# Performance work log

Hardware: AMD Instinct MI355X
Metric: run time of the kernel (lower is better)

## Reference

```python
import jax, jax.numpy as jnp
import numpy as np


def _lstm(x, W_ih, W_hh, b_ih, b_hh):
    """PyTorch-convention LSTM. x: [B, T, I] -> (ys [B, T, H], h_T [B, H]).
    Gate order i, f, g, o as in torch.nn.LSTM."""
    def step(carry, xt):
        h, c = carry
        gates = xt @ W_ih.T + b_ih + h @ W_hh.T + b_hh
        i, f, g, o = jnp.split(gates, 4, axis=-1)
        c = jax.nn.sigmoid(f) * c + jax.nn.sigmoid(i) * jnp.tanh(g)
        h = jax.nn.sigmoid(o) * jnp.tanh(c)
        return (h, c), h
    B = x.shape[0]
    H = W_hh.shape[1]
    init = (jnp.zeros((B, H), x.dtype), jnp.zeros((B, H), x.dtype))
    (hT, _), ys = jax.lax.scan(step, init, jnp.swapaxes(x, 0, 1))
    return jnp.swapaxes(ys, 0, 1), hT


def setup_inputs():
    key = jax.random.key(0)
    ks = jax.random.split(key, 13)
    B, S, F = 256, 1024, 16
    p = lambda k, shape: jax.random.normal(k, shape, jnp.float32) * 0.1
    return {
        "x": jax.random.normal(ks[0], (B, S, F), jnp.float32),
        "data": 0,
        "W_ih1": p(ks[1], (32, 1)),  "W_hh1": p(ks[2], (32, 8)),
        "b_ih1": p(ks[3], (32,)),    "b_hh1": p(ks[4], (32,)),
        "W_ih2": p(ks[5], (512, 8)), "W_hh2": p(ks[6], (512, 128)),
        "b_ih2": p(ks[7], (512,)),   "b_hh2": p(ks[8], (512,)),
        "W1": p(ks[9], (64, 128)),   "b1": p(ks[10], (64,)),
        "W2": p(ks[11], (1, 64)),    "b2": p(ks[12], (1,)),
    }


def reference(x, data, W_ih1, W_hh1, b_ih1, b_hh1,
              W_ih2, W_hh2, b_ih2, b_hh2, W1, b1, W2, b2):
    B, S, F = x.shape
    # rnn1: original loops over batch; here all B*S rows are one big batch of
    # length-F sequences with feature dim 1. We only need the final hidden h_T.
    x1 = x.reshape(B * S, F, 1)
    _, h1 = _lstm(x1, W_ih1, W_hh1, b_ih1, b_hh1)            # [B*S, 8]
    # original does .detach().numpy() -> gradient is cut here
    h1 = jax.lax.stop_gradient(h1).reshape(B, S, 8)
    ys2, _ = _lstm(h1, W_ih2, W_hh2, b_ih2, b_hh2)           # [B, S, 128]
    last = ys2[:, -1, :]                                     # [B, 128]
    return (last @ W1.T + b1) @ W2.T + b2                    # [B, 1]
```

## Files before the change

kernel.cpp:

```cpp
#include <hip/hip_runtime.h>
#include <cstdint>

typedef _Float16 f16x2 __attribute__((ext_vector_type(2)));

#define L2E 1.44269504f

__device__ __forceinline__ float sig2(float y) {
  return __builtin_amdgcn_rcpf(1.f + exp2f(-y));
}
__device__ __forceinline__ float tanhc(float c) {
  return fmaf(2.f, __builtin_amdgcn_rcpf(1.f + exp2f(c * (-2.f * L2E))), -1.f);
}
__device__ __forceinline__ int packf16(float a, float b) {
  f16x2 p; p.x = (_Float16)a; p.y = (_Float16)b;
  return __builtin_bit_cast(int, p);
}
__device__ __forceinline__ float dot2(int w, int h, float acc) {
  return __builtin_amdgcn_fdot2(__builtin_bit_cast(f16x2, w),
                                __builtin_bit_cast(f16x2, h), acc, false);
}
template <int CTRL>
__device__ __forceinline__ float qp(float v) {
  return __int_as_float(__builtin_amdgcn_update_dpp(
      0, __float_as_int(v), CTRL, 0xF, 0xF, true));
}
#define QP_X1 0xB1

__global__ __launch_bounds__(256, 1) void fused_kernel(
    const float* __restrict__ x, const float* __restrict__ Wih1,
    const float* __restrict__ Whh1, const float* __restrict__ bih1,
    const float* __restrict__ bhh1, const float* __restrict__ Wih2,
    const float* __restrict__ Whh2, const float* __restrict__ bih2,
    const float* __restrict__ bhh2, const float* __restrict__ Wd1,
    const float* __restrict__ bd1, const float* __restrict__ Wd2,
    const float* __restrict__ bd2, float* __restrict__ out) {
  __shared__ __align__(16) int4 sX[1026];
  __shared__ __align__(16) _Float16 sH[2][128];

  const int b = blockIdx.x;
  const int t = threadIdx.x;

  {
    int whh2[128];
#pragma unroll
    for (int r = 0; r < 32; ++r) {
      const float s = (r >> 3) == 2 ? 2.f * L2E : L2E;
#pragma unroll
      for (int j = 0; j < 4; ++j) {
        float2 v = ((const float2*)(Whh1 + r * 8))[j];
        whh2[r * 4 + j] = packf16(v.x * s, v.y * s);
      }
    }
    int wxb[32];
#pragma unroll
    for (int r = 0; r < 32; ++r) {
      const float s = (r >> 3) == 2 ? 2.f * L2E : L2E;
      wxb[r] = packf16(Wih1[r] * s, (bih1[r] + bhh1[r]) * s);
    }
#pragma unroll
    for (int i = 0; i < 128; i += 8)
      asm volatile("" : "+v"(whh2[i]), "+v"(whh2[i + 1]), "+v"(whh2[i + 2]),
                        "+v"(whh2[i + 3]), "+v"(whh2[i + 4]), "+v"(whh2[i + 5]),
                        "+v"(whh2[i + 6]), "+v"(whh2[i + 7]));

#pragma unroll 1
    for (int ch = 0; ch < 4; ++ch) {
      const int c = ch * 256 + t;
      const float* __restrict__ xp = x + ((size_t)b * 1024 + c) * 16;
      float cc[8];
      int h2[4];
#pragma unroll
      for (int k = 0; k < 8; ++k) cc[k] = 0.f;
#pragma unroll
      for (int j = 0; j < 4; ++j) h2[j] = 0;

      float xv = xp[0];
#pragma unroll 1
      for (int u = 0; u < 16; ++u) {
        float xnl = xp[(u + 1) & 15];
        const int xt1 = packf16(xv, 1.f);
        float hn[8];
#pragma unroll
        for (int k = 0; k < 8; ++k) {
          float acc[4];
#pragma unroll
          for (int gi = 0; gi < 4; ++gi) {
            const int r = gi * 8 + k;
            float a = dot2(wxb[r], xt1, 0.f);
            a = dot2(whh2[r * 4 + 0], h2[0], a);
            a = dot2(whh2[r * 4 + 1], h2[1], a);
            a = dot2(whh2[r * 4 + 2], h2[2], a);
            a = dot2(whh2[r * 4 + 3], h2[3], a);
            acc[gi] = a;
          }
          float iv = sig2(acc[0]), fv = sig2(acc[1]);
          float gv = fmaf(2.f, sig2(acc[2]), -1.f), ov = sig2(acc[3]);
          cc[k] = fmaf(fv, cc[k], iv * gv);
          hn[k] = ov * tanhc(cc[k]);
        }
#pragma unroll
        for (int j = 0; j < 4; ++j) h2[j] = packf16(hn[2 * j], hn[2 * j + 1]);
        xv = xnl;
      }
      int4 o;
      o.x = h2[0]; o.y = h2[1]; o.z = h2[2]; o.w = h2[3];
      sX[c] = o;
    }
  }

  const int m = t >> 1;
  const int q = t & 1;
  const bool isq1 = (q == 1);

  int w[128];
#pragma unroll
  for (int g = 0; g < 4; ++g) {
    const float s = (g == 2) ? 2.f * L2E : L2E;
    const float2* p = (const float2*)(Whh2 + (size_t)(g * 128 + m) * 128 + q * 64);
#pragma unroll
    for (int j = 0; j < 32; ++j) {
      float2 v = p[j];
      w[g * 32 + j] = packf16(v.x * s, v.y * s);
    }
  }
#pragma unroll
  for (int i = 0; i < 128; i += 8)
    asm volatile("" : "+v"(w[i]), "+v"(w[i + 1]), "+v"(w[i + 2]),
                      "+v"(w[i + 3]), "+v"(w[i + 4]), "+v"(w[i + 5]),
                      "+v"(w[i + 6]), "+v"(w[i + 7]));

  int wigA[4], wigB[4];
  float biasA, biasB;
  {
    const int gA = 2 * q, gB = 2 * q + 1;
    const float sa = (gA == 2) ? 2.f * L2E : L2E;
    const float sb = L2E;
    const int rowA = gA * 128 + m;
    const int rowB = gB * 128 + m;
    const float2* pa = (const float2*)(Wih2 + (size_t)rowA * 8);
    const float2* pb = (const float2*)(Wih2 + (size_t)rowB * 8);
#pragma unroll
    for (int j = 0; j < 4; ++j) {
      float2 va = pa[j], vb = pb[j];
      wigA[j] = packf16(va.x * sa, va.y * sa);
      wigB[j] = packf16(vb.x * sb, vb.y * sb);
    }
    biasA = (bih2[rowA] + bhh2[rowA]) * sa;
    biasB = (bih2[rowB] + bhh2[rowB]) * sb;
  }

  int hq[32];
#pragma unroll
  for (int i = 0; i < 32; ++i) hq[i] = 0;
  float c = 0.f;

  __syncthreads();
  int4 xc = sX[0];

#define LSTM2_STEP(BUF, NEXT_IDX)                                          \
  {                                                                        \
    float bxA = biasA, bxB = biasB;                                        \
    bxA = dot2(wigA[0], xc.x, bxA);                                        \
    bxA = dot2(wigA[1], xc.y, bxA);                                        \
    bxA = dot2(wigA[2], xc.z, bxA);                                        \
    bxA = dot2(wigA[3], xc.w, bxA);                                        \
    bxB = dot2(wigB[0], xc.x, bxB);                                        \
    bxB = dot2(wigB[1], xc.y, bxB);                                        \
    bxB = dot2(wigB[2], xc.z, bxB);                                        \
    bxB = dot2(wigB[3], xc.w, bxB);                                        \
    float R0a = 0.f, R1a = 0.f, R2a = 0.f, R3a = 0.f;                      \
    float R0b = 0.f, R1b = 0.f, R2b = 0.f, R3b = 0.f;                      \
    _Pragma("unroll")                                                      \
    for (int j = 0; j < 16; ++j) {                                         \
      R0a = dot2(w[j], hq[j], R0a);                                        \
      R1a = dot2(w[32 + j], hq[j], R1a);                                   \
      R2a = dot2(w[64 + j], hq[j], R2a);                                   \
      R3a = dot2(w[96 + j], hq[j], R3a);                                   \
    }                                                                      \
    _Pragma("unroll")                                                      \
    for (int j = 16; j < 32; ++j) {                                        \
      R0b = dot2(w[j], hq[j], R0b);                                        \
      R1b = dot2(w[32 + j], hq[j], R1b);                                   \
      R2b = dot2(w[64 + j], hq[j], R2b);                                   \
      R3b = dot2(w[96 + j], hq[j], R3b);                                   \
    }                                                                      \
    float R0 = R0a + R0b, R1 = R1a + R1b;                                  \
    float R2 = R2a + R2b, R3 = R3a + R3b;                                  \
    float vA = isq1 ? R0 : R2;                                             \
    float Sa = (isq1 ? R2 : R0) + qp<QP_X1>(vA) + bxA;                     \
    float vB = isq1 ? R1 : R3;                                             \
    float Sb = (isq1 ? R3 : R1) + qp<QP_X1>(vB) + bxB;                     \
    float sga = sig2(Sa);                                                  \
    float actA = isq1 ? fmaf(2.f, sga, -1.f) : sga;                        \
    float actB = sig2(Sb);                                                 \
    float ga = qp<QP_X1>(actA);                                            \
    float gb = qp<QP_X1>(actB);                                            \
    float iv = isq1 ? ga : actA;                                           \
    float gv = isq1 ? actA : ga;                                           \
    float fv = isq1 ? gb : actB;                                           \
    float ov = isq1 ? actB : gb;                                           \
    c = fmaf(fv, c, iv * gv);                                              \
    float hx = ov * tanhc(c);                                              \
    if (!isq1) sH[BUF][m] = (_Float16)hx;                                  \
    __syncthreads();                                                       \
    const int4* src = (const int4*)(&sH[BUF][q * 64]);                     \
    int4 A = src[0], Bv = src[1], C = src[2], D = src[3];                  \
    int4 E = src[4], F = src[5], G2 = src[6], H = src[7];                  \
    hq[0] = A.x;   hq[1] = A.y;   hq[2] = A.z;   hq[3] = A.w;              \
    hq[4] = Bv.x;  hq[5] = Bv.y;  hq[6] = Bv.z;  hq[7] = Bv.w;             \
    hq[8] = C.x;   hq[9] = C.y;   hq[10] = C.z;  hq[11] = C.w;             \
    hq[12] = D.x;  hq[13] = D.y;  hq[14] = D.z;  hq[15] = D.w;             \
    hq[16] = E.x;  hq[17] = E.y;  hq[18] = E.z;  hq[19] = E.w;             \
    hq[20] = F.x;  hq[21] = F.y;  hq[22] = F.z;  hq[23] = F.w;             \
    hq[24] = G2.x; hq[25] = G2.y; hq[26] = G2.z; hq[27] = G2.w;            \
    hq[28] = H.x;  hq[29] = H.y;  hq[30] = H.z;  hq[31] = H.w;             \
    xc = sX[NEXT_IDX];                                                     \
  }

#pragma unroll 1
  for (int ts2 = 0; ts2 < 512; ++ts2) {
    LSTM2_STEP(0, 2 * ts2 + 1)
    LSTM2_STEP(1, 2 * ts2 + 2)
  }
#undef LSTM2_STEP

  if (t < 64) {
    float a = bd1[t];
#pragma unroll
    for (int k = 0; k < 128; ++k)
      a = fmaf(Wd1[t * 128 + k], (float)sH[1][k], a);
    float v = a * Wd2[t];
#pragma unroll
    for (int off = 32; off > 0; off >>= 1) v += __shfl_down(v, off);
    if (t == 0) out[b] = v + bd2[0];
  }
}

extern "C" void kernel_launch(void* const* d_in, const int* in_sizes, int n_in,
                              void* d_out, int out_size, void* d_ws, size_t ws_size,
                              hipStream_t stream) {
  const float* x    = (const float*)d_in[0];
  const float* Wih1 = (const float*)d_in[2];
  const float* Whh1 = (const float*)d_in[3];
  const float* bih1 = (const float*)d_in[4];
  const float* bhh1 = (const float*)d_in[5];
  const float* Wih2 = (const float*)d_in[6];
  const float* Whh2 = (const float*)d_in[7];
  const float* bih2 = (const float*)d_in[8];
  const float* bhh2 = (const float*)d_in[9];
  const float* W1   = (const float*)d_in[10];
  const float* b1   = (const float*)d_in[11];
  const float* W2   = (const float*)d_in[12];
  const float* b2   = (const float*)d_in[13];
  float* out = (float*)d_out;

  fused_kernel<<<256, 256, 0, stream>>>(x, Wih1, Whh1, bih1, bhh1,
                                        Wih2, Whh2, bih2, bhh2,
                                        W1, b1, W2, b2, out);
}
```

Baseline: 659.3 us.

## Pack two batch sequences per 512-thread block, halving the grid

Each block now processes two batch elements with 512 threads, each 256-thread half running its own LSTM2 recurrence on separate shared-memory buffers. The grid shrinks from 256 to 128 blocks. The aim is better use of each CU, since 256 blocks on a 256-CU device left one wave group per CU and latency-bound. The risk is that the shared __syncthreads now couples both halves across all 512 threads, so every step's barrier costs more and one half can stall the other.

Measured after the change: 1.081 ms. 1.64x slower.

```diff
diff --git a/kernel.cpp b/kernel.cpp
--- a/kernel.cpp
+++ b/kernel.cpp
@@ -26,7 +26,7 @@
 }
 #define QP_X1 0xB1
 
-__global__ __launch_bounds__(256, 1) void fused_kernel(
+__global__ __launch_bounds__(512, 1) void fused_kernel(
     const float* __restrict__ x, const float* __restrict__ Wih1,
     const float* __restrict__ Whh1, const float* __restrict__ bih1,
     const float* __restrict__ bhh1, const float* __restrict__ Wih2,
@@ -34,8 +34,8 @@
     const float* __restrict__ bhh2, const float* __restrict__ Wd1,
     const float* __restrict__ bd1, const float* __restrict__ Wd2,
     const float* __restrict__ bd2, float* __restrict__ out) {
-  __shared__ __align__(16) int4 sX[1026];
-  __shared__ __align__(16) _Float16 sH[2][128];
+  __shared__ __align__(16) int4 sX2[2][1026];
+  __shared__ __align__(16) _Float16 sH2[2][2][128];
 
   const int b = blockIdx.x;
   const int t = threadIdx.x;
@@ -65,8 +65,8 @@
 
 #pragma unroll 1
     for (int ch = 0; ch < 4; ++ch) {
-      const int c = ch * 256 + t;
-      const float* __restrict__ xp = x + ((size_t)b * 1024 + c) * 16;
+      const int c = ch * 512 + t;
+      const float* __restrict__ xp = x + ((size_t)b * 2048 + c) * 16;
       float cc[8];
       int h2[4];
 #pragma unroll
@@ -104,12 +104,14 @@
       }
       int4 o;
       o.x = h2[0]; o.y = h2[1]; o.z = h2[2]; o.w = h2[3];
-      sX[c] = o;
-    }
-  }
-
-  const int m = t >> 1;
-  const int q = t & 1;
+      sX2[c >> 10][c & 1023] = o;
+    }
+  }
+
+  const int sq = t >> 8;
+  const int tl = t & 255;
+  const int m = tl >> 1;
+  const int q = tl & 1;
   const bool isq1 = (q == 1);
 
   int w[128];
@@ -154,8 +156,11 @@
   for (int i = 0; i < 32; ++i) hq[i] = 0;
   float c = 0.f;
 
+  const int4* __restrict__ sXs = sX2[sq];
+  _Float16 (* __restrict__ sHs)[128] = sH2[sq];
+
   __syncthreads();
-  int4 xc = sX[0];
+  int4 xc = sXs[0];
 
 #define LSTM2_STEP(BUF, NEXT_IDX)                                          \
   {                                                                        \
@@ -201,9 +206,9 @@
     float ov = isq1 ? actB : gb;                                           \
     c = fmaf(fv, c, iv * gv);                                              \
     float hx = ov * tanhc(c);                                              \
-    if (!isq1) sH[BUF][m] = (_Float16)hx;                                  \
+    if (!isq1) sHs[BUF][m] = (_Float16)hx;                                 \
     __syncthreads();                                                       \
-    const int4* src = (const int4*)(&sH[BUF][q * 64]);                     \
+    const int4* src = (const int4*)(&sHs[BUF][q * 64]);                    \
     int4 A = src[0], Bv = src[1], C = src[2], D = src[3];                  \
     int4 E = src[4], F = src[5], G2 = src[6], H = src[7];                  \
     hq[0] = A.x;   hq[1] = A.y;   hq[2] = A.z;   hq[3] = A.w;              \
@@ -214,7 +219,7 @@
     hq[20] = F.x;  hq[21] = F.y;  hq[22] = F.z;  hq[23] = F.w;             \
     hq[24] = G2.x; hq[25] = G2.y; hq[26] = G2.z; hq[27] = G2.w;            \
     hq[28] = H.x;  hq[29] = H.y;  hq[30] = H.z;  hq[31] = H.w;             \
-    xc = sX[NEXT_IDX];                                                     \
+    xc = sXs[NEXT_IDX];                                                    \
   }
 
 #pragma unroll 1
@@ -224,15 +229,15 @@
   }
 #undef LSTM2_STEP
 
-  if (t < 64) {
-    float a = bd1[t];
+  if (tl < 64) {
+    float a = bd1[tl];
 #pragma unroll
     for (int k = 0; k < 128; ++k)
-      a = fmaf(Wd1[t * 128 + k], (float)sH[1][k], a);
-    float v = a * Wd2[t];
+      a = fmaf(Wd1[tl * 128 + k], (float)sHs[1][k], a);
+    float v = a * Wd2[tl];
 #pragma unroll
     for (int off = 32; off > 0; off >>= 1) v += __shfl_down(v, off);
-    if (t == 0) out[b] = v + bd2[0];
+    if (tl == 0) out[2 * b + sq] = v + bd2[0];
   }
 }
 
@@ -254,7 +259,7 @@
   const float* b2   = (const float*)d_in[13];
   float* out = (float*)d_out;
 
-  fused_kernel<<<256, 256, 0, stream>>>(x, Wih1, Whh1, bih1, bhh1,
+  fused_kernel<<<128, 512, 0, stream>>>(x, Wih1, Whh1, bih1, bhh1,
                                         Wih2, Whh2, bih2, bhh2,
                                         W1, b1, W2, b2, out);
 }
```

## Split LSTM2 hidden units across 4 lanes with fp32 FMA and 512 threads

Applied to the files above, without the earlier changes.

Doubles the block to 512 threads. Each hidden unit of the second LSTM is now handled by 4 lanes, each covering 32 of the 128 hidden inputs for all four gates, with a two-level DPP quad reduction and an exchange of the gate values. The packed fp16 dot2 path is replaced by fp32 FMAs, and h and the layer-1 outputs are stored in shared memory as fp32. This halves the serial per-step dot work on each lane, at the cost of more shuffles, a larger block taking part in each barrier, and more LDS traffic. Layer 1 now runs in 2 chunks instead of 4.

New measurement: 832.0 us. 26.2% more time.

```diff
diff --git a/kernel.cpp b/kernel.cpp
--- a/kernel.cpp
+++ b/kernel.cpp
@@ -25,8 +25,9 @@
       0, __float_as_int(v), CTRL, 0xF, 0xF, true));
 }
 #define QP_X1 0xB1
-
-__global__ __launch_bounds__(256, 1) void fused_kernel(
+#define QP_X2 0x4E
+
+__global__ __launch_bounds__(512, 2) void fused_kernel(
     const float* __restrict__ x, const float* __restrict__ Wih1,
     const float* __restrict__ Whh1, const float* __restrict__ bih1,
     const float* __restrict__ bhh1, const float* __restrict__ Wih2,
@@ -34,8 +35,8 @@
     const float* __restrict__ bhh2, const float* __restrict__ Wd1,
     const float* __restrict__ bd1, const float* __restrict__ Wd2,
     const float* __restrict__ bd2, float* __restrict__ out) {
-  __shared__ __align__(16) int4 sX[1026];
-  __shared__ __align__(16) _Float16 sH[2][128];
+  __shared__ __align__(16) float sXf[1026][8];
+  __shared__ __align__(16) float sHf[2][128];
 
   const int b = blockIdx.x;
   const int t = threadIdx.x;
@@ -64,8 +65,8 @@
                         "+v"(whh2[i + 6]), "+v"(whh2[i + 7]));
 
 #pragma unroll 1
-    for (int ch = 0; ch < 4; ++ch) {
-      const int c = ch * 256 + t;
+    for (int ch = 0; ch < 2; ++ch) {
+      const int c = ch * 512 + t;
       const float* __restrict__ xp = x + ((size_t)b * 1024 + c) * 16;
       float cc[8];
       int h2[4];
@@ -74,12 +75,12 @@
 #pragma unroll
       for (int j = 0; j < 4; ++j) h2[j] = 0;
 
+      float hn[8];
       float xv = xp[0];
 #pragma unroll 1
       for (int u = 0; u < 16; ++u) {
         float xnl = xp[(u + 1) & 15];
         const int xt1 = packf16(xv, 1.f);
-        float hn[8];
 #pragma unroll
         for (int k = 0; k < 8; ++k) {
           float acc[4];
@@ -102,25 +103,34 @@
         for (int j = 0; j < 4; ++j) h2[j] = packf16(hn[2 * j], hn[2 * j + 1]);
         xv = xnl;
       }
-      int4 o;
-      o.x = h2[0]; o.y = h2[1]; o.z = h2[2]; o.w = h2[3];
-      sX[c] = o;
-    }
-  }
-
-  const int m = t >> 1;
-  const int q = t & 1;
+      float4* dst = (float4*)sXf[c];
+      float4 o0, o1;
+      o0.x = hn[0]; o0.y = hn[1]; o0.z = hn[2]; o0.w = hn[3];
+      o1.x = hn[4]; o1.y = hn[5]; o1.z = hn[6]; o1.w = hn[7];
+      dst[0] = o0; dst[1] = o1;
+    }
+  }
+
+  const int m = t >> 2;
+  const int q = t & 3;
+  const int G = ((q & 1) << 1) | (q >> 1);
+  const bool sel0 = (q & 1) != 0;
+  const bool sel1 = (q & 2) != 0;
+  const bool isq0 = (q == 0);
   const bool isq1 = (q == 1);
 
-  int w[128];
+  float w[128];
 #pragma unroll
   for (int g = 0; g < 4; ++g) {
     const float s = (g == 2) ? 2.f * L2E : L2E;
-    const float2* p = (const float2*)(Whh2 + (size_t)(g * 128 + m) * 128 + q * 64);
-#pragma unroll
-    for (int j = 0; j < 32; ++j) {
-      float2 v = p[j];
-      w[g * 32 + j] = packf16(v.x * s, v.y * s);
+    const float4* p = (const float4*)(Whh2 + (size_t)(g * 128 + m) * 128 + q * 32);
+#pragma unroll
+    for (int j = 0; j < 8; ++j) {
+      float4 v = p[j];
+      w[g * 32 + 4 * j + 0] = v.x * s;
+      w[g * 32 + 4 * j + 1] = v.y * s;
+      w[g * 32 + 4 * j + 2] = v.z * s;
+      w[g * 32 + 4 * j + 3] = v.w * s;
     }
   }
 #pragma unroll
@@ -129,83 +139,81 @@
                       "+v"(w[i + 3]), "+v"(w[i + 4]), "+v"(w[i + 5]),
                       "+v"(w[i + 6]), "+v"(w[i + 7]));
 
-  int wigA[4], wigB[4];
-  float biasA, biasB;
+  float wig[8];
+  float bias;
   {
-    const int gA = 2 * q, gB = 2 * q + 1;
-    const float sa = (gA == 2) ? 2.f * L2E : L2E;
-    const float sb = L2E;
-    const int rowA = gA * 128 + m;
-    const int rowB = gB * 128 + m;
-    const float2* pa = (const float2*)(Wih2 + (size_t)rowA * 8);
-    const float2* pb = (const float2*)(Wih2 + (size_t)rowB * 8);
-#pragma unroll
-    for (int j = 0; j < 4; ++j) {
-      float2 va = pa[j], vb = pb[j];
-      wigA[j] = packf16(va.x * sa, va.y * sa);
-      wigB[j] = packf16(vb.x * sb, vb.y * sb);
-    }
-    biasA = (bih2[rowA] + bhh2[rowA]) * sa;
-    biasB = (bih2[rowB] + bhh2[rowB]) * sb;
-  }
-
-  int hq[32];
-#pragma unroll
-  for (int i = 0; i < 32; ++i) hq[i] = 0;
+    const float s = (G == 2) ? 2.f * L2E : L2E;
+    const float4* pi = (const float4*)(Wih2 + (size_t)(G * 128 + m) * 8);
+    float4 a = pi[0], bv = pi[1];
+    wig[0] = a.x * s;  wig[1] = a.y * s;  wig[2] = a.z * s;  wig[3] = a.w * s;
+    wig[4] = bv.x * s; wig[5] = bv.y * s; wig[6] = bv.z * s; wig[7] = bv.w * s;
+    bias = (bih2[G * 128 + m] + bhh2[G * 128 + m]) * s;
+  }
+
+  float hq[32];
+#pragma unroll
+  for (int i = 0; i < 32; ++i) hq[i] = 0.f;
   float c = 0.f;
 
   __syncthreads();
-  int4 xc = sX[0];
+  float4 xc0 = ((const float4*)sXf[0])[0];
+  float4 xc1 = ((const float4*)sXf[0])[1];
 
 #define LSTM2_STEP(BUF, NEXT_IDX)                                          \
   {                                                                        \
-    float bxA = biasA, bxB = biasB;                                        \
-    bxA = dot2(wigA[0], xc.x, bxA);                                        \
-    bxA = dot2(wigA[1], xc.y, bxA);                                        \
-    bxA = dot2(wigA[2], xc.z, bxA);                                        \
-    bxA = dot2(wigA[3], xc.w, bxA);                                        \
-    bxB = dot2(wigB[0], xc.x, bxB);                                        \
-    bxB = dot2(wigB[1], xc.y, bxB);                                        \
-    bxB = dot2(wigB[2], xc.z, bxB);                                        \
-    bxB = dot2(wigB[3], xc.w, bxB);                                        \
+    float bx = bias;                                                       \
+    bx = fmaf(wig[0], xc0.x, bx);                                          \
+    bx = fmaf(wig[1], xc0.y, bx);                                          \
+    bx = fmaf(wig[2], xc0.z, bx);                                          \
+    bx = fmaf(wig[3], xc0.w, bx);                                          \
+    bx = fmaf(wig[4], xc1.x, bx);                                          \
+    bx = fmaf(wig[5], xc1.y, bx);                                          \
+    bx = fmaf(wig[6], xc1.z, bx);                                          \
+    bx = fmaf(wig[7], xc1.w, bx);                                          \
     float R0a = 0.f, R1a = 0.f, R2a = 0.f, R3a = 0.f;                      \
     float R0b = 0.f, R1b = 0.f, R2b = 0.f, R3b = 0.f;                      \
     _Pragma("unroll")                                                      \
     for (int j = 0; j < 16; ++j) {                                         \
-      R0a = dot2(w[j], hq[j], R0a);                                        \
-      R1a = dot2(w[32 + j], hq[j], R1a);                                   \
-      R2a = dot2(w[64 + j], hq[j], R2a);                                   \
-      R3a = dot2(w[96 + j], hq[j], R3a);                                   \
+      R0a = fmaf(w[j], hq[j], R0a);                                        \
+      R1a = fmaf(w[32 + j], hq[j], R1a);                                   \
+      R2a = fmaf(w[64 + j], hq[j], R2a);                                   \
+      R3a = fmaf(w[96 + j], hq[j], R3a);                                   \
     }                                                                      \
     _Pragma("unroll")                                                      \
     for (int j = 16; j < 32; ++j) {                                        \
-      R0b = dot2(w[j], hq[j], R0b);                                        \
-      R1b = dot2(w[32 + j], hq[j], R1b);                                   \
-      R2b = dot2(w[64 + j], hq[j], R2b);                                   \
-      R3b = dot2(w[96 + j], hq[j], R3b);                                   \
+      R0b = fmaf(w[j], hq[j], R0b);                                        \
+      R1b = fmaf(w[32 + j], hq[j], R1b);                                   \
+      R2b = fmaf(w[64 + j], hq[j], R2b);                                   \
+      R3b = fmaf(w[96 + j], hq[j], R3b);                                   \
     }                                                                      \
     float R0 = R0a + R0b, R1 = R1a + R1b;                                  \
     float R2 = R2a + R2b, R3 = R3a + R3b;                                  \
-    float vA = isq1 ? R0 : R2;                                             \
-    float Sa = (isq1 ? R2 : R0) + qp<QP_X1>(vA) + bxA;                     \
-    float vB = isq1 ? R1 : R3;                                             \
-    float Sb = (isq1 ? R3 : R1) + qp<QP_X1>(vB) + bxB;                     \
-    float sga = sig2(Sa);                                                  \
-    float actA = isq1 ? fmaf(2.f, sga, -1.f) : sga;                        \
-    float actB = sig2(Sb);                                                 \
-    float ga = qp<QP_X1>(actA);                                            \
-    float gb = qp<QP_X1>(actB);                                            \
-    float iv = isq1 ? ga : actA;                                           \
-    float gv = isq1 ? actA : ga;                                           \
-    float fv = isq1 ? gb : actB;                                           \
-    float ov = isq1 ? actB : gb;                                           \
+    float s0 = sel0 ? R0 : R2, s1 = sel0 ? R1 : R3;                        \
+    float k0 = sel0 ? R2 : R0, k1 = sel0 ? R3 : R1;                        \
+    float S0 = k0 + qp<QP_X1>(s0);                                         \
+    float S1 = k1 + qp<QP_X1>(s1);                                         \
+    float s2 = sel1 ? S0 : S1;                                             \
+    float k2 = sel1 ? S1 : S0;                                             \
+    float S = k2 + qp<QP_X2>(s2) + bx;                                     \
+    float sg = sig2(S);                                                    \
+    float act = isq1 ? fmaf(2.f, sg, -1.f) : sg;                           \
+    float v0 = act;                                                        \
+    float v1 = qp<QP_X1>(v0);                                              \
+    float v2 = qp<QP_X2>(v0);                                              \
+    float v3 = qp<QP_X2>(v1);                                              \
+    float p01 = sel0 ? v1 : v0, p23 = sel0 ? v3 : v2;                      \
+    float q01 = sel0 ? v0 : v1, q23 = sel0 ? v2 : v3;                      \
+    float iv = sel1 ? p23 : p01;                                           \
+    float fv = sel1 ? p01 : p23;                                           \
+    float gv = sel1 ? q23 : q01;                                           \
+    float ov = sel1 ? q01 : q23;                                           \
     c = fmaf(fv, c, iv * gv);                                              \
     float hx = ov * tanhc(c);                                              \
-    if (!isq1) sH[BUF][m] = (_Float16)hx;                                  \
+    if (isq0) sHf[BUF][m] = hx;                                            \
     __syncthreads();                                                       \
-    const int4* src = (const int4*)(&sH[BUF][q * 64]);                     \
-    int4 A = src[0], Bv = src[1], C = src[2], D = src[3];                  \
-    int4 E = src[4], F = src[5], G2 = src[6], H = src[7];                  \
+    const float4* src = (const float4*)(&sHf[BUF][q * 32]);                \
+    float4 A = src[0], Bv = src[1], C = src[2], D = src[3];                \
+    float4 E = src[4], F = src[5], G2 = src[6], H = src[7];                \
     hq[0] = A.x;   hq[1] = A.y;   hq[2] = A.z;   hq[3] = A.w;              \
     hq[4] = Bv.x;  hq[5] = Bv.y;  hq[6] = Bv.z;  hq[7] = Bv.w;             \
     hq[8] = C.x;   hq[9] = C.y;   hq[10] = C.z;  hq[11] = C.w;             \
@@ -214,7 +222,8 @@
     hq[20] = F.x;  hq[21] = F.y;  hq[22] = F.z;  hq[23] = F.w;             \
     hq[24] = G2.x; hq[25] = G2.y; hq[26] = G2.z; hq[27] = G2.w;            \
     hq[28] = H.x;  hq[29] = H.y;  hq[30] = H.z;  hq[31] = H.w;             \
-    xc = sX[NEXT_IDX];                                                     \
+    xc0 = ((const float4*)sXf[NEXT_IDX])[0];                               \
+    xc1 = ((const float4*)sXf[NEXT_IDX])[1];                               \
   }
 
 #pragma unroll 1
@@ -228,7 +237,7 @@
     float a = bd1[t];
 #pragma unroll
     for (int k = 0; k < 128; ++k)
-      a = fmaf(Wd1[t * 128 + k], (float)sH[1][k], a);
+      a = fmaf(Wd1[t * 128 + k], sHf[1][k], a);
     float v = a * Wd2[t];
 #pragma unroll
     for (int off = 32; off > 0; off >>= 1) v += __shfl_down(v, off);
@@ -254,7 +263,7 @@
   const float* b2   = (const float*)d_in[13];
   float* out = (float*)d_out;
 
-  fused_kernel<<<256, 256, 0, stream>>>(x, Wih1, Whh1, bih1, bhh1,
+  fused_kernel<<<256, 512, 0, stream>>>(x, Wih1, Whh1, bih1, bhh1,
                                         Wih2, Whh2, bih2, bhh2,
                                         W1, b1, W2, b2, out);
 }
```

## Compute second LSTM recurrence with MFMA 16x16x32 f16 instead of fdot2

Applied to the files above, without the earlier changes.

The second LSTM's recurrent and input matvec moves from per-thread packed fdot2 chains onto MFMA 16x16x32 f16 instructions. The hidden state sits in row 0 of the A operand, and input and bias are folded into a fifth MFMA per gate tile. Each wave owns 32 hidden units across 8 gate tiles, and 16 lanes per wave do the pointwise gate math. This removes the DPP quad-pair exchanges and the large scalar dot-product issue count. In exchange, 15 of the 16 MFMA rows do no useful work, and each step now has 40 dependent-chain MFMAs per wave plus narrower pointwise work.

New measurement: 842.3 us. +27.8%, slower.

```diff
diff --git a/kernel.cpp b/kernel.cpp
--- a/kernel.cpp
+++ b/kernel.cpp
@@ -2,6 +2,8 @@
 #include <cstdint>
 
 typedef _Float16 f16x2 __attribute__((ext_vector_type(2)));
+typedef _Float16 f16x8v __attribute__((ext_vector_type(8)));
+typedef float f32x4v __attribute__((ext_vector_type(4)));
 
 #define L2E 1.44269504f
 
@@ -19,12 +21,6 @@
   return __builtin_amdgcn_fdot2(__builtin_bit_cast(f16x2, w),
                                 __builtin_bit_cast(f16x2, h), acc, false);
 }
-template <int CTRL>
-__device__ __forceinline__ float qp(float v) {
-  return __int_as_float(__builtin_amdgcn_update_dpp(
-      0, __float_as_int(v), CTRL, 0xF, 0xF, true));
-}
-#define QP_X1 0xB1
 
 __global__ __launch_bounds__(256, 1) void fused_kernel(
     const float* __restrict__ x, const float* __restrict__ Wih1,
@@ -34,8 +30,8 @@
     const float* __restrict__ bhh2, const float* __restrict__ Wd1,
     const float* __restrict__ bd1, const float* __restrict__ Wd2,
     const float* __restrict__ bd2, float* __restrict__ out) {
-  __shared__ __align__(16) int4 sX[1026];
-  __shared__ __align__(16) _Float16 sH[2][128];
+  __shared__ __align__(16) int4 sXi[1025];
+  __shared__ __align__(16) _Float16 sHh[2][128];
 
   const int b = blockIdx.x;
   const int t = threadIdx.x;
@@ -104,117 +100,116 @@
       }
       int4 o;
       o.x = h2[0]; o.y = h2[1]; o.z = h2[2]; o.w = h2[3];
-      sX[c] = o;
-    }
-  }
-
-  const int m = t >> 1;
-  const int q = t & 1;
-  const bool isq1 = (q == 1);
-
-  int w[128];
-#pragma unroll
-  for (int g = 0; g < 4; ++g) {
+      sXi[c] = o;
+    }
+  }
+
+  const int w = t >> 6;
+  const int lane = t & 63;
+  const int lc = lane & 15;
+  const int lk = lane >> 4;
+
+  f16x8v bh[4][8];
+  f16x8v bx[8];
+#pragma unroll
+  for (int nt = 0; nt < 8; ++nt) {
+    const int g = nt >> 1;
+    const int row = g * 128 + w * 32 + (nt & 1) * 16 + lc;
     const float s = (g == 2) ? 2.f * L2E : L2E;
-    const float2* p = (const float2*)(Whh2 + (size_t)(g * 128 + m) * 128 + q * 64);
-#pragma unroll
-    for (int j = 0; j < 32; ++j) {
-      float2 v = p[j];
-      w[g * 32 + j] = packf16(v.x * s, v.y * s);
-    }
-  }
-#pragma unroll
-  for (int i = 0; i < 128; i += 8)
-    asm volatile("" : "+v"(w[i]), "+v"(w[i + 1]), "+v"(w[i + 2]),
-                      "+v"(w[i + 3]), "+v"(w[i + 4]), "+v"(w[i + 5]),
-                      "+v"(w[i + 6]), "+v"(w[i + 7]));
-
-  int wigA[4], wigB[4];
-  float biasA, biasB;
-  {
-    const int gA = 2 * q, gB = 2 * q + 1;
-    const float sa = (gA == 2) ? 2.f * L2E : L2E;
-    const float sb = L2E;
-    const int rowA = gA * 128 + m;
-    const int rowB = gB * 128 + m;
-    const float2* pa = (const float2*)(Wih2 + (size_t)rowA * 8);
-    const float2* pb = (const float2*)(Wih2 + (size_t)rowB * 8);
-#pragma unroll
-    for (int j = 0; j < 4; ++j) {
-      float2 va = pa[j], vb = pb[j];
-      wigA[j] = packf16(va.x * sa, va.y * sa);
-      wigB[j] = packf16(vb.x * sb, vb.y * sb);
-    }
-    biasA = (bih2[rowA] + bhh2[rowA]) * sa;
-    biasB = (bih2[rowB] + bhh2[rowB]) * sb;
-  }
-
-  int hq[32];
-#pragma unroll
-  for (int i = 0; i < 32; ++i) hq[i] = 0;
-  float c = 0.f;
+#pragma unroll
+    for (int kt = 0; kt < 4; ++kt) {
+      const float* p = Whh2 + (size_t)row * 128 + kt * 32 + lk * 8;
+      f16x8v f;
+#pragma unroll
+      for (int i = 0; i < 8; ++i) f[i] = (_Float16)(p[i] * s);
+      bh[kt][nt] = f;
+    }
+    f16x8v fx = {};
+    if (lk == 0) {
+      const float* px = Wih2 + (size_t)row * 8;
+#pragma unroll
+      for (int i = 0; i < 8; ++i) fx[i] = (_Float16)(px[i] * s);
+    } else if (lk == 1) {
+      fx[0] = (_Float16)((bih2[row] + bhh2[row]) * s);
+    }
+    bx[nt] = fx;
+  }
+
+  f16x8v xb1 = {};
+  if (lc == 0 && lk == 1) xb1[0] = (_Float16)1.f;
+
+  f16x8v ah0 = {}, ah1 = {}, ah2 = {}, ah3 = {};
+  float cst0 = 0.f, cst1 = 0.f;
 
   __syncthreads();
-  int4 xc = sX[0];
-
-#define LSTM2_STEP(BUF, NEXT_IDX)                                          \
-  {                                                                        \
-    float bxA = biasA, bxB = biasB;                                        \
-    bxA = dot2(wigA[0], xc.x, bxA);                                        \
-    bxA = dot2(wigA[1], xc.y, bxA);                                        \
-    bxA = dot2(wigA[2], xc.z, bxA);                                        \
-    bxA = dot2(wigA[3], xc.w, bxA);                                        \
-    bxB = dot2(wigB[0], xc.x, bxB);                                        \
-    bxB = dot2(wigB[1], xc.y, bxB);                                        \
-    bxB = dot2(wigB[2], xc.z, bxB);                                        \
-    bxB = dot2(wigB[3], xc.w, bxB);                                        \
-    float R0a = 0.f, R1a = 0.f, R2a = 0.f, R3a = 0.f;                      \
-    float R0b = 0.f, R1b = 0.f, R2b = 0.f, R3b = 0.f;                      \
-    _Pragma("unroll")                                                      \
-    for (int j = 0; j < 16; ++j) {                                         \
-      R0a = dot2(w[j], hq[j], R0a);                                        \
-      R1a = dot2(w[32 + j], hq[j], R1a);                                   \
-      R2a = dot2(w[64 + j], hq[j], R2a);                                   \
-      R3a = dot2(w[96 + j], hq[j], R3a);                                   \
-    }                                                                      \
-    _Pragma("unroll")                                                      \
-    for (int j = 16; j < 32; ++j) {                                        \
-      R0b = dot2(w[j], hq[j], R0b);                                        \
-      R1b = dot2(w[32 + j], hq[j], R1b);                                   \
-      R2b = dot2(w[64 + j], hq[j], R2b);                                   \
-      R3b = dot2(w[96 + j], hq[j], R3b);                                   \
-    }                                                                      \
-    float R0 = R0a + R0b, R1 = R1a + R1b;                                  \
-    float R2 = R2a + R2b, R3 = R3a + R3b;                                  \
-    float vA = isq1 ? R0 : R2;                                             \
-    float Sa = (isq1 ? R2 : R0) + qp<QP_X1>(vA) + bxA;                     \
-    float vB = isq1 ? R1 : R3;                                             \
-    float Sb = (isq1 ? R3 : R1) + qp<QP_X1>(vB) + bxB;                     \
-    float sga = sig2(Sa);                                                  \
-    float actA = isq1 ? fmaf(2.f, sga, -1.f) : sga;                        \
-    float actB = sig2(Sb);                                                 \
-    float ga = qp<QP_X1>(actA);                                            \
-    float gb = qp<QP_X1>(actB);                                            \
-    float iv = isq1 ? ga : actA;                                           \
-    float gv = isq1 ? actA : ga;                                           \
-    float fv = isq1 ? gb : actB;                                           \
-    float ov = isq1 ? actB : gb;                                           \
-    c = fmaf(fv, c, iv * gv);                                              \
-    float hx = ov * tanhc(c);                                              \
-    if (!isq1) sH[BUF][m] = (_Float16)hx;                                  \
-    __syncthreads();                                                       \
-    const int4* src = (const int4*)(&sH[BUF][q * 64]);                     \
-    int4 A = src[0], Bv = src[1], C = src[2], D = src[3];                  \
-    int4 E = src[4], F = src[5], G2 = src[6], H = src[7];                  \
-    hq[0] = A.x;   hq[1] = A.y;   hq[2] = A.z;   hq[3] = A.w;              \
-    hq[4] = Bv.x;  hq[5] = Bv.y;  hq[6] = Bv.z;  hq[7] = Bv.w;             \
-    hq[8] = C.x;   hq[9] = C.y;   hq[10] = C.z;  hq[11] = C.w;             \
-    hq[12] = D.x;  hq[13] = D.y;  hq[14] = D.z;  hq[15] = D.w;             \
-    hq[16] = E.x;  hq[17] = E.y;  hq[18] = E.z;  hq[19] = E.w;             \
-    hq[20] = F.x;  hq[21] = F.y;  hq[22] = F.z;  hq[23] = F.w;             \
-    hq[24] = G2.x; hq[25] = G2.y; hq[26] = G2.z; hq[27] = G2.w;            \
-    hq[28] = H.x;  hq[29] = H.y;  hq[30] = H.z;  hq[31] = H.w;             \
-    xc = sX[NEXT_IDX];                                                     \
+  int4 xr_cur = sXi[0];
+
+#define LSTM2_STEP(BUF, NEXTI)                                               \
+  {                                                                          \
+    f16x8v xa = (lc == 0 && lk == 0)                                         \
+                    ? __builtin_bit_cast(f16x8v, xr_cur) : xb1;              \
+    f32x4v acc0 = {}, acc1 = {}, acc2 = {}, acc3 = {};                       \
+    f32x4v acc4 = {}, acc5 = {}, acc6 = {}, acc7 = {};                       \
+    acc0 = __builtin_amdgcn_mfma_f32_16x16x32_f16(ah0, bh[0][0], acc0, 0, 0, 0); \
+    acc0 = __builtin_amdgcn_mfma_f32_16x16x32_f16(ah1, bh[1][0], acc0, 0, 0, 0); \
+    acc0 = __builtin_amdgcn_mfma_f32_16x16x32_f16(ah2, bh[2][0], acc0, 0, 0, 0); \
+    acc0 = __builtin_amdgcn_mfma_f32_16x16x32_f16(ah3, bh[3][0], acc0, 0, 0, 0); \
+    acc0 = __builtin_amdgcn_mfma_f32_16x16x32_f16(xa, bx[0], acc0, 0, 0, 0); \
+    acc1 = __builtin_amdgcn_mfma_f32_16x16x32_f16(ah0, bh[0][1], acc1, 0, 0, 0); \
+    acc1 = __builtin_amdgcn_mfma_f32_16x16x32_f16(ah1, bh[1][1], acc1, 0, 0, 0); \
+    acc1 = __builtin_amdgcn_mfma_f32_16x16x32_f16(ah2, bh[2][1], acc1, 0, 0, 0); \
+    acc1 = __builtin_amdgcn_mfma_f32_16x16x32_f16(ah3, bh[3][1], acc1, 0, 0, 0); \
+    acc1 = __builtin_amdgcn_mfma_f32_16x16x32_f16(xa, bx[1], acc1, 0, 0, 0); \
+    acc2 = __builtin_amdgcn_mfma_f32_16x16x32_f16(ah0, bh[0][2], acc2, 0, 0, 0); \
+    acc2 = __builtin_amdgcn_mfma_f32_16x16x32_f16(ah1, bh[1][2], acc2, 0, 0, 0); \
+    acc2 = __builtin_amdgcn_mfma_f32_16x16x32_f16(ah2, bh[2][2], acc2, 0, 0, 0); \
+    acc2 = __builtin_amdgcn_mfma_f32_16x16x32_f16(ah3, bh[3][2], acc2, 0, 0, 0); \
+    acc2 = __builtin_amdgcn_mfma_f32_16x16x32_f16(xa, bx[2], acc2, 0, 0, 0); \
+    acc3 = __builtin_amdgcn_mfma_f32_16x16x32_f16(ah0, bh[0][3], acc3, 0, 0, 0); \
+    acc3 = __builtin_amdgcn_mfma_f32_16x16x32_f16(ah1, bh[1][3], acc3, 0, 0, 0); \
+    acc3 = __builtin_amdgcn_mfma_f32_16x16x32_f16(ah2, bh[2][3], acc3, 0, 0, 0); \
+    acc3 = __builtin_amdgcn_mfma_f32_16x16x32_f16(ah3, bh[3][3], acc3, 0, 0, 0); \
+    acc3 = __builtin_amdgcn_mfma_f32_16x16x32_f16(xa, bx[3], acc3, 0, 0, 0); \
+    acc4 = __builtin_amdgcn_mfma_f32_16x16x32_f16(ah0, bh[0][4], acc4, 0, 0, 0); \
+    acc4 = __builtin_amdgcn_mfma_f32_16x16x32_f16(ah1, bh[1][4], acc4, 0, 0, 0); \
+    acc4 = __builtin_amdgcn_mfma_f32_16x16x32_f16(ah2, bh[2][4], acc4, 0, 0, 0); \
+    acc4 = __builtin_amdgcn_mfma_f32_16x16x32_f16(ah3, bh[3][4], acc4, 0, 0, 0); \
+    acc4 = __builtin_amdgcn_mfma_f32_16x16x32_f16(xa, bx[4], acc4, 0, 0, 0); \
+    acc5 = __builtin_amdgcn_mfma_f32_16x16x32_f16(ah0, bh[0][5], acc5, 0, 0, 0); \
+    acc5 = __builtin_amdgcn_mfma_f32_16x16x32_f16(ah1, bh[1][5], acc5, 0, 0, 0); \
+    acc5 = __builtin_amdgcn_mfma_f32_16x16x32_f16(ah2, bh[2][5], acc5, 0, 0, 0); \
+    acc5 = __builtin_amdgcn_mfma_f32_16x16x32_f16(ah3, bh[3][5], acc5, 0, 0, 0); \
+    acc5 = __builtin_amdgcn_mfma_f32_16x16x32_f16(xa, bx[5], acc5, 0, 0, 0); \
+    acc6 = __builtin_amdgcn_mfma_f32_16x16x32_f16(ah0, bh[0][6], acc6, 0, 0, 0); \
+    acc6 = __builtin_amdgcn_mfma_f32_16x16x32_f16(ah1, bh[1][6], acc6, 0, 0, 0); \
+    acc6 = __builtin_amdgcn_mfma_f32_16x16x32_f16(ah2, bh[2][6], acc6, 0, 0, 0); \
+    acc6 = __builtin_amdgcn_mfma_f32_16x16x32_f16(ah3, bh[3][6], acc6, 0, 0, 0); \
+    acc6 = __builtin_amdgcn_mfma_f32_16x16x32_f16(xa, bx[6], acc6, 0, 0, 0); \
+    acc7 = __builtin_amdgcn_mfma_f32_16x16x32_f16(ah0, bh[0][7], acc7, 0, 0, 0); \
+    acc7 = __builtin_amdgcn_mfma_f32_16x16x32_f16(ah1, bh[1][7], acc7, 0, 0, 0); \
+    acc7 = __builtin_amdgcn_mfma_f32_16x16x32_f16(ah2, bh[2][7], acc7, 0, 0, 0); \
+    acc7 = __builtin_amdgcn_mfma_f32_16x16x32_f16(ah3, bh[3][7], acc7, 0, 0, 0); \
+    acc7 = __builtin_amdgcn_mfma_f32_16x16x32_f16(xa, bx[7], acc7, 0, 0, 0); \
+    \
+    if (lane < 16) {                                                         \
+      float iv0 = sig2(acc0[0]), fv0 = sig2(acc2[0]);                        \
+      float gv0 = fmaf(2.f, sig2(acc4[0]), -1.f), ov0 = sig2(acc6[0]);       \
+      cst0 = fmaf(fv0, cst0, iv0 * gv0);                                     \
+      sHh[BUF][w * 32 + lane] = (_Float16)(ov0 * tanhc(cst0));               \
+      float iv1 = sig2(acc1[0]), fv1 = sig2(acc3[0]);                        \
+      float gv1 = fmaf(2.f, sig2(acc5[0]), -1.f), ov1 = sig2(acc7[0]);       \
+      cst1 = fmaf(fv1, cst1, iv1 * gv1);                                     \
+      sHh[BUF][w * 32 + 16 + lane] = (_Float16)(ov1 * tanhc(cst1));          \
+    }                                                                        \
+    __syncthreads();                                                         \
+    if (lc == 0) {                                                           \
+      const int4* hb = (const int4*)sHh[BUF];                                \
+      ah0 = __builtin_bit_cast(f16x8v, hb[0 + lk]);                          \
+      ah1 = __builtin_bit_cast(f16x8v, hb[4 + lk]);                          \
+      ah2 = __builtin_bit_cast(f16x8v, hb[8 + lk]);                          \
+      ah3 = __builtin_bit_cast(f16x8v, hb[12 + lk]);                         \
+    }                                                                        \
+    xr_cur = sXi[NEXTI];                                                     \
   }
 
 #pragma unroll 1
@@ -228,7 +223,7 @@
     float a = bd1[t];
 #pragma unroll
     for (int k = 0; k < 128; ++k)
-      a = fmaf(Wd1[t * 128 + k], (float)sH[1][k], a);
+      a = fmaf(Wd1[t * 128 + k], (float)sHh[1][k], a);
     float v = a * Wd2[t];
 #pragma unroll
     for (int off = 32; off > 0; off >>= 1) v += __shfl_down(v, off);
```
